# Performance work log

Measured on AMD Instinct MI355X. Metric: run time of the kernel, lower is better.

Reference implementation:

```python
import jax, jax.numpy as jnp
import numpy as np

DIM = 1024
HEADS = 16
HEAD_DIM = DIM // HEADS
NUM_FILTERS = 4
NUM_TAPS = 101
RES = 512

def setup_inputs() -> dict:
    key = jax.random.key(0)
    ks = jax.random.split(key, 5)
    B, S = 2, 2048
    x = jax.random.normal(ks[0], (B, S, DIM), dtype=jnp.float32)
    Wqkv = jax.random.normal(ks[1], (3 * DIM, DIM), dtype=jnp.float32) * (DIM ** -0.5)
    Wout = jax.random.normal(ks[2], (DIM, DIM), dtype=jnp.float32) * (DIM ** -0.5)
    Wpos = jax.random.normal(ks[3], (HEADS, NUM_FILTERS), dtype=jnp.float32) * 0.5
    coeffs = jax.random.normal(ks[4], (NUM_FILTERS, NUM_TAPS), dtype=jnp.float32) * 0.05
    return {"x": x, "Wqkv": Wqkv, "Wout": Wout, "Wpos": Wpos, "coeffs": coeffs}

def _fir_fft(c, sig):
    # c: (T,), sig: (R,) -> causal FFT convolution, first R samples
    R = sig.shape[0]
    L = R + c.shape[0] - 1
    out = jnp.fft.ifft(jnp.fft.fft(sig, n=L) * jnp.fft.fft(c, n=L)).real
    return out[:R]

def reference(x, Wqkv, Wout, Wpos, coeffs):
    B, S, D = x.shape
    scale = HEAD_DIM ** -0.5

    # filtered prototype table: (R, F)
    proto = jnp.linspace(0.0, 1.0, RES).astype(x.dtype)
    table = jax.vmap(_fir_fft, in_axes=(0, None))(coeffs, proto).T  # (R, F)

    # relative-distance index matrix (S, S), constants derived from static shape
    r = jnp.arange(S)
    rel = jnp.abs(r[None, :] - r[:, None]).astype(jnp.float32) / max(S - 1, 1)
    idx = jnp.clip(jnp.round(rel * (RES - 1)).astype(jnp.int32), 0, RES - 1)

    pos_feat = table[idx]                                   # (S, S, F)
    pos_bias = jnp.einsum('ijf,hf->hij', pos_feat, Wpos)    # (H, S, S)

    qkv = jnp.einsum('bsd,ed->bse', x, Wqkv)                # (B, S, 3D)
    q, k, v = jnp.split(qkv, 3, axis=-1)
    q = q.reshape(B, S, HEADS, HEAD_DIM)
    k = k.reshape(B, S, HEADS, HEAD_DIM)
    v = v.reshape(B, S, HEADS, HEAD_DIM)

    logits = jnp.einsum('bihd,bjhd->bhij', q, k) * scale + pos_bias[None]
    attn = jax.nn.softmax(logits, axis=-1)
    out = jnp.einsum('bhij,bjhd->bihd', attn, v).reshape(B, S, D)
    return jnp.einsum('bsd,ed->bse', out, Wout)
```

## Files before the change

### kernel.cpp

```cpp
#include <hip/hip_runtime.h>
#include <hip/hip_bf16.h>
#include <cstddef>

#define SEQ     2048
#define BATCH   2
#define DIMSZ   1024
#define HEADS   16
#define HDIM    64
#define E3      3072
#define RESN    512
#define NTAPS   101
#define NFILT   4
#define MROWS   (BATCH * SEQ)
#define LOG2E   1.44269504088896340736f

typedef __attribute__((ext_vector_type(8))) short bf16x8;
typedef __attribute__((ext_vector_type(4))) float f32x4;

__device__ __forceinline__ unsigned short f2bf(float f) {
  unsigned u = __float_as_uint(f);
  u += 0x7fffu + ((u >> 16) & 1u);
  return (unsigned short)(u >> 16);
}
__device__ __forceinline__ float bf2f(unsigned short h) {
  return __uint_as_float(((unsigned)h) << 16);
}
__device__ __forceinline__ void split2(float f, unsigned short& h, unsigned short& l) {
  h = f2bf(f);
  l = f2bf(f - bf2f(h));
}
__device__ __forceinline__ unsigned pkbf(float a, float b) {
  __hip_bfloat162 t = __float22bfloat162_rn(float2{a, b});
  union { __hip_bfloat162 h; unsigned u; } cv; cv.h = t;
  return cv.u;
}
__device__ __forceinline__ void async16(void* lds, const void* g) {
  __builtin_amdgcn_global_load_lds(
      (const __attribute__((address_space(1))) unsigned int*)g,
      (__attribute__((address_space(3))) unsigned int*)lds, 16, 0, 0);
}
#define EXP2(x) __builtin_amdgcn_exp2f(x)

__global__ __launch_bounds__(256) void cvt_bf16_kern(
    const float* __restrict__ src, unsigned short* __restrict__ dst, int n)
{
  const int i = (blockIdx.x * 256 + threadIdx.x) * 8;
  if (i >= n) return;
  const float4 a = *(const float4*)(src + i);
  const float4 b = *(const float4*)(src + i + 4);
  ushort4 p = {f2bf(a.x), f2bf(a.y), f2bf(a.z), f2bf(a.w)};
  ushort4 q = {f2bf(b.x), f2bf(b.y), f2bf(b.z), f2bf(b.w)};
  *(ushort4*)(dst + i)     = p;
  *(ushort4*)(dst + i + 4) = q;
}

__global__ __launch_bounds__(256) void split_pair_kern(
    const float* __restrict__ src, unsigned short* __restrict__ hi,
    unsigned short* __restrict__ lo, int n)
{
  const int i = (blockIdx.x * 256 + threadIdx.x) * 4;
  if (i >= n) return;
  const float4 a = *(const float4*)(src + i);
  ushort4 h, l;
  split2(a.x, h.x, l.x); split2(a.y, h.y, l.y);
  split2(a.z, h.z, l.z); split2(a.w, h.w, l.w);
  *(ushort4*)(hi + i) = h;
  *(ushort4*)(lo + i) = l;
}

__global__ __launch_bounds__(256) void pbias_kernel(
    const float* __restrict__ coeffs, const float* __restrict__ Wpos,
    float* __restrict__ pbias2)
{
  __shared__ float table[RESN][NFILT];
  const int h = blockIdx.x;
  const int tid = threadIdx.x;
  for (int rf = tid; rf < RESN * NFILT; rf += 256) {
    const int r = rf >> 2, f = rf & 3;
    const int tmax = r < (NTAPS - 1) ? r : (NTAPS - 1);
    float s = 0.f;
    for (int t = 0; t <= tmax; ++t)
      s += coeffs[f * NTAPS + t] * ((float)(r - t) * (1.0f / (float)(RESN - 1)));
    table[r][f] = s;
  }
  __syncthreads();
  float wp[NFILT];
#pragma unroll
  for (int f = 0; f < NFILT; ++f) wp[f] = Wpos[h * NFILT + f];
  for (int d = tid; d < SEQ; d += 256) {
    const float rel = (float)d / (float)(SEQ - 1);
    int idx = (int)rintf(rel * (float)(RESN - 1));
    idx = idx < 0 ? 0 : (idx > RESN - 1 ? RESN - 1 : idx);
    float s = 0.f;
#pragma unroll
    for (int f = 0; f < NFILT; ++f) s += table[idx][f] * wp[f];
    pbias2[h * SEQ + d] = s * LOG2E;
  }
}

__global__ __launch_bounds__(256, 4) void gemm_bf16(
    const unsigned short* __restrict__ A, const unsigned short* __restrict__ B,
    unsigned short* __restrict__ C, int M, int N, int K)
{
  __shared__ unsigned short As[2][128][32];
  __shared__ unsigned short Bs[2][128][32];
  const int tid = threadIdx.x;
  const int lane = tid & 63;
  const int w = tid >> 6, wm = w >> 1, wn = w & 1;
  const int c = lane & 15, G = lane >> 4;

  const int nwg = gridDim.x * gridDim.y;
  const int bid = blockIdx.y * gridDim.x + blockIdx.x;
  const int swz = (bid & 7) * (nwg >> 3) + (bid >> 3);
  const int bx = swz % gridDim.x, by = swz / gridDim.x;
  const int m0 = by * 128, n0 = bx * 128;

  const int srow = lane >> 2;
  const int scol = (lane & 3) << 3;
  const unsigned short* Ab = A + (size_t)m0 * K;
  const unsigned short* Bb = B + (size_t)n0 * K;

  f32x4 acc[4][4];
#pragma unroll
  for (int mf = 0; mf < 4; ++mf)
#pragma unroll
    for (int nf = 0; nf < 4; ++nf) acc[mf][nf] = (f32x4){0.f, 0.f, 0.f, 0.f};

  auto stage = [&](int buf, int k0) {
#pragma unroll
    for (int r = 0; r < 2; ++r) {
      const int chunk = r * 4 + w;
      const int row = (chunk << 4) + srow;
      async16(&As[buf][chunk << 4][0], Ab + (size_t)row * K + k0 + scol);
      async16(&Bs[buf][chunk << 4][0], Bb + (size_t)row * K + k0 + scol);
    }
  };

  stage(0, 0);
  __syncthreads();
  int cur = 0;
  const int NT = K >> 5;
  for (int t = 0; t < NT; ++t) {
    if (t + 1 < NT) stage(cur ^ 1, (t + 1) << 5);
    bf16x8 fa[4], fb[4];
#pragma unroll
    for (int mf = 0; mf < 4; ++mf)
      fa[mf] = *(const bf16x8*)&As[cur][wm * 64 + 16 * mf + c][8 * G];
#pragma unroll
    for (int nf = 0; nf < 4; ++nf)
      fb[nf] = *(const bf16x8*)&Bs[cur][wn * 64 + 16 * nf + c][8 * G];
#pragma unroll
    for (int nf = 0; nf < 4; ++nf)
#pragma unroll
      for (int mf = 0; mf < 4; ++mf)
        acc[mf][nf] = __builtin_amdgcn_mfma_f32_16x16x32_bf16(fa[mf], fb[nf], acc[mf][nf], 0, 0, 0);
    __syncthreads();
    cur ^= 1;
  }

#pragma unroll
  for (int mf = 0; mf < 4; ++mf)
#pragma unroll
    for (int nf = 0; nf < 4; ++nf)
#pragma unroll
      for (int r = 0; r < 4; ++r)
        C[(size_t)(m0 + wm * 64 + 16 * mf + 4 * G + r) * N + n0 + wn * 64 + 16 * nf + c] =
            f2bf(acc[mf][nf][r]);
}

__global__ __launch_bounds__(256, 4) void gemm_split3(
    const unsigned short* __restrict__ Ah, const unsigned short* __restrict__ Al,
    const unsigned short* __restrict__ Bh, const unsigned short* __restrict__ Bl,
    float* __restrict__ C, int M, int N, int K)
{
  __shared__ unsigned short AhS[2][64][32], AlS[2][64][32];
  __shared__ unsigned short BhS[2][64][32], BlS[2][64][32];
  const int tid = threadIdx.x;
  const int lane = tid & 63;
  const int w = tid >> 6, wm = w >> 1, wn = w & 1;
  const int c = lane & 15, G = lane >> 4;

  const int nwg = gridDim.x * gridDim.y;
  const int bid = blockIdx.y * gridDim.x + blockIdx.x;
  const int swz = (bid & 7) * (nwg >> 3) + (bid >> 3);
  const int bx = swz % gridDim.x, by = swz / gridDim.x;
  const int m0 = by * 64, n0 = bx * 64;

  const int srow = lane >> 2;
  const int scol = (lane & 3) << 3;

  f32x4 acc[2][2];
#pragma unroll
  for (int mf = 0; mf < 2; ++mf)
#pragma unroll
    for (int nf = 0; nf < 2; ++nf) acc[mf][nf] = (f32x4){0.f, 0.f, 0.f, 0.f};

  auto stage = [&](int buf, int k0) {
    const int arow = m0 + 16 * w + srow;
    const int brow = n0 + 16 * w + srow;
    async16(&AhS[buf][16 * w][0], Ah + (size_t)arow * K + k0 + scol);
    async16(&AlS[buf][16 * w][0], Al + (size_t)arow * K + k0 + scol);
    async16(&BhS[buf][16 * w][0], Bh + (size_t)brow * K + k0 + scol);
    async16(&BlS[buf][16 * w][0], Bl + (size_t)brow * K + k0 + scol);
  };

  stage(0, 0);
  __syncthreads();
  int cur = 0;
  const int NT = K >> 5;
  for (int t = 0; t < NT; ++t) {
    if (t + 1 < NT) stage(cur ^ 1, (t + 1) << 5);
    bf16x8 fah[2], fal[2], fbh[2], fbl[2];
#pragma unroll
    for (int mf = 0; mf < 2; ++mf) {
      fah[mf] = *(const bf16x8*)&AhS[cur][32 * wm + 16 * mf + c][8 * G];
      fal[mf] = *(const bf16x8*)&AlS[cur][32 * wm + 16 * mf + c][8 * G];
    }
#pragma unroll
    for (int nf = 0; nf < 2; ++nf) {
      fbh[nf] = *(const bf16x8*)&BhS[cur][32 * wn + 16 * nf + c][8 * G];
      fbl[nf] = *(const bf16x8*)&BlS[cur][32 * wn + 16 * nf + c][8 * G];
    }
#pragma unroll
    for (int nf = 0; nf < 2; ++nf)
#pragma unroll
      for (int mf = 0; mf < 2; ++mf) {
        acc[mf][nf] = __builtin_amdgcn_mfma_f32_16x16x32_bf16(fah[mf], fbh[nf], acc[mf][nf], 0, 0, 0);
        acc[mf][nf] = __builtin_amdgcn_mfma_f32_16x16x32_bf16(fah[mf], fbl[nf], acc[mf][nf], 0, 0, 0);
        acc[mf][nf] = __builtin_amdgcn_mfma_f32_16x16x32_bf16(fal[mf], fbh[nf], acc[mf][nf], 0, 0, 0);
      }
    __syncthreads();
    cur ^= 1;
  }

#pragma unroll
  for (int mf = 0; mf < 2; ++mf)
#pragma unroll
    for (int nf = 0; nf < 2; ++nf)
#pragma unroll
      for (int r = 0; r < 4; ++r)
        C[(size_t)(m0 + 32 * wm + 16 * mf + 4 * G + r) * N + n0 + 32 * wn + 16 * nf + c] =
            acc[mf][nf][r];
}

__global__ __launch_bounds__(256, 4) void attn_pure(
    const unsigned short* __restrict__ qkv,
    const float* __restrict__ pbias2,
    unsigned short* __restrict__ ao_hi,
    unsigned short* __restrict__ ao_lo)
{
  __shared__ unsigned short Kh[64][64];
  __shared__ unsigned short Vh[64][64];
  __shared__ unsigned short Ps[64][64];
  __shared__ float pb[SEQ];

  const int tid = threadIdx.x;
  const int lane = tid & 63;
  const int w = tid >> 6;
  const int c = lane & 15, G = lane >> 4;
  const int bh = blockIdx.y, b = bh >> 4, h = bh & 15;
  const int i0 = blockIdx.x * 64;
  const int i_glob = i0 + w * 16 + c;
  const float scale2 = 0.125f * LOG2E;

  for (int idx = tid * 4; idx < SEQ; idx += 1024)
    *(float4*)&pb[idx] = *(const float4*)(pbias2 + h * SEQ + idx);

  bf16x8 qb[2];
#pragma unroll
  for (int ks = 0; ks < 2; ++ks)
    qb[ks] = *(const bf16x8*)(qkv + (size_t)(b * SEQ + i_glob) * E3 + h * HDIM + 32 * ks + 8 * G);

  f32x4 oacc[4];
#pragma unroll
  for (int nf = 0; nf < 4; ++nf) oacc[nf] = (f32x4){0.f, 0.f, 0.f, 0.f};
  float mi = -1e30f, li = 0.f;

  const int vd8 = 8 * (tid & 7);
  const int vjp = 2 * (tid >> 3);
  const int klrow = lane >> 3;
  const int klsl  = lane & 7;

  for (int jt = 0; jt < SEQ / 64; ++jt) {
    const int j0 = jt * 64;
    const size_t rowK = (size_t)(b * SEQ + j0) * E3 + DIMSZ + h * HDIM;
    const size_t rowV = (size_t)(b * SEQ + j0) * E3 + 2 * DIMSZ + h * HDIM;

    const bf16x8 v0 = *(const bf16x8*)(qkv + rowV + (size_t)vjp * E3 + vd8);
    const bf16x8 v1 = *(const bf16x8*)(qkv + rowV + (size_t)(vjp + 1) * E3 + vd8);

    __syncthreads();

#pragma unroll
    for (int r = 0; r < 2; ++r) {
      const int chunk = r * 4 + w;
      const int krow = (chunk << 3) + klrow;
      const int ksl = klsl ^ (krow & 7);
      async16(&Kh[chunk << 3][0], qkv + rowK + (size_t)krow * E3 + 8 * ksl);
    }
#pragma unroll
    for (int e = 0; e < 8; ++e) {
      const int d = vd8 + e;
      const unsigned pk = (unsigned)(unsigned short)v0[e] |
                          ((unsigned)(unsigned short)v1[e] << 16);
      const int col = (((vjp >> 3) ^ (d & 7)) << 3) | (vjp & 7);
      *(unsigned*)&Vh[d][col] = pk;
    }
    __syncthreads();

    f32x4 st[4];
#pragma unroll
    for (int mf = 0; mf < 4; ++mf) st[mf] = (f32x4){0.f, 0.f, 0.f, 0.f};
#pragma unroll
    for (int ks = 0; ks < 2; ++ks)
#pragma unroll
      for (int mf = 0; mf < 4; ++mf) {
        const int sr = (4 * ks + G) ^ (c & 7);
        const bf16x8 ka = *(const bf16x8*)&Kh[16 * mf + c][8 * sr];
        st[mf] = __builtin_amdgcn_mfma_f32_16x16x32_bf16(ka, qb[ks], st[mf], 0, 0, 0);
      }

    float p[16];
    float rm = -1e30f;
#pragma unroll
    for (int mf = 0; mf < 4; ++mf)
#pragma unroll
      for (int r = 0; r < 4; ++r) {
        const int j = j0 + 16 * mf + 4 * G + r;
        const int d = i_glob > j ? i_glob - j : j - i_glob;
        const float lg = fmaf(st[mf][r], scale2, pb[d]);
        p[mf * 4 + r] = lg;
        rm = fmaxf(rm, lg);
      }
    rm = fmaxf(rm, __shfl_xor(rm, 16));
    rm = fmaxf(rm, __shfl_xor(rm, 32));
    const float newm = fmaxf(mi, rm);
    const float fr = EXP2(mi - newm);
    float rs = 0.f;
#pragma unroll
    for (int t = 0; t < 16; ++t) {
      p[t] = EXP2(p[t] - newm);
      rs += p[t];
    }
    rs += __shfl_xor(rs, 16);
    rs += __shfl_xor(rs, 32);
    li = li * fr + rs;
    mi = newm;
    float frr[4];
#pragma unroll
    for (int r = 0; r < 4; ++r) frr[r] = __shfl(fr, 20 * G + r);
#pragma unroll
    for (int nf = 0; nf < 4; ++nf)
#pragma unroll
      for (int r = 0; r < 4; ++r) oacc[nf][r] *= frr[r];

#pragma unroll
    for (int mf = 0; mf < 4; ++mf) {
      const int sw = (2 * mf + (G >> 1)) ^ (c & 7);
      uint2 pw = {pkbf(p[4 * mf + 0], p[4 * mf + 1]),
                  pkbf(p[4 * mf + 2], p[4 * mf + 3])};
      *(uint2*)&Ps[16 * w + c][8 * sw + 4 * (G & 1)] = pw;
    }

#pragma unroll
    for (int ks = 0; ks < 2; ++ks) {
      const int spr = (4 * ks + G) ^ (c & 7);
      const bf16x8 pa = *(const bf16x8*)&Ps[16 * w + c][8 * spr];
#pragma unroll
      for (int nf = 0; nf < 4; ++nf) {
        const int d = 16 * nf + c;
        const int sv = (4 * ks + G) ^ (d & 7);
        const bf16x8 vb = *(const bf16x8*)&Vh[d][8 * sv];
        oacc[nf] = __builtin_amdgcn_mfma_f32_16x16x32_bf16(pa, vb, oacc[nf], 0, 0, 0);
      }
    }
  }

  float rinv[4];
#pragma unroll
  for (int r = 0; r < 4; ++r) rinv[r] = 1.0f / __shfl(li, 20 * G + r);
#pragma unroll
  for (int nf = 0; nf < 4; ++nf)
#pragma unroll
    for (int r = 0; r < 4; ++r) {
      const float v = oacc[nf][r] * rinv[r];
      const size_t off = (size_t)(b * SEQ + i0 + 16 * w + 4 * G + r) * DIMSZ +
                         h * HDIM + 16 * nf + c;
      unsigned short vh, vl;
      split2(v, vh, vl);
      ao_hi[off] = vh;
      ao_lo[off] = vl;
    }
}

extern "C" void kernel_launch(void* const* d_in, const int* in_sizes, int n_in,
                              void* d_out, int out_size, void* d_ws, size_t ws_size,
                              hipStream_t stream) {
  const float* x      = (const float*)d_in[0];
  const float* Wqkv   = (const float*)d_in[1];
  const float* Wout   = (const float*)d_in[2];
  const float* Wpos   = (const float*)d_in[3];
  const float* coeffs = (const float*)d_in[4];
  float* out = (float*)d_out;

  unsigned short* qkv_bf  = (unsigned short*)d_ws;
  unsigned short* x_bf    = qkv_bf + (size_t)MROWS * E3;
  unsigned short* wqkv_bf = x_bf + (size_t)MROWS * DIMSZ;
  unsigned short* wout_h  = wqkv_bf + (size_t)E3 * DIMSZ;
  unsigned short* wout_l  = wout_h + (size_t)DIMSZ * DIMSZ;
  unsigned short* ao_h    = wout_l + (size_t)DIMSZ * DIMSZ;
  unsigned short* ao_l    = ao_h + (size_t)MROWS * DIMSZ;
  float* pbias2 = (float*)(ao_l + (size_t)MROWS * DIMSZ);

  const int nx = MROWS * DIMSZ;
  const int nw = E3 * DIMSZ;
  const int no = DIMSZ * DIMSZ;

  cvt_bf16_kern<<<nx / 2048, 256, 0, stream>>>(x, x_bf, nx);
  cvt_bf16_kern<<<nw / 2048, 256, 0, stream>>>(Wqkv, wqkv_bf, nw);
  split_pair_kern<<<no / 1024, 256, 0, stream>>>(Wout, wout_h, wout_l, no);
  pbias_kernel<<<HEADS, 256, 0, stream>>>(coeffs, Wpos, pbias2);

  dim3 g1(E3 / 128, MROWS / 128);
  gemm_bf16<<<g1, 256, 0, stream>>>(x_bf, wqkv_bf, qkv_bf, MROWS, E3, DIMSZ);

  dim3 g2(SEQ / 64, BATCH * HEADS);
  attn_pure<<<g2, 256, 0, stream>>>(qkv_bf, pbias2, ao_h, ao_l);

  dim3 g3(DIMSZ / 64, MROWS / 64);
  gemm_split3<<<g3, 256, 0, stream>>>(ao_h, ao_l, wout_h, wout_l, out, MROWS, DIMSZ, DIMSZ);
}
```

Before: 318.1 us.

## Enlarge output GEMM tile, keep P in registers, lazy softmax rescale

The output projection GEMM now uses 128x64 tiles, so each B fragment load is reused across four M fragments. The attention kernel drops the shared P buffer and repacks P into MFMA A-operand layout with permlane swaps. It also skips the online-softmax rescale when the running max grows by no more than 8, reads the position bias directly from global memory instead of staging it in LDS, and swizzles the block order. These changes aim to cut LDS traffic, syncs and rescale ALU work, at the cost of more registers and uncached gather loads of the bias.

```diff
diff --git a/kernel.cpp b/kernel.cpp
--- a/kernel.cpp
+++ b/kernel.cpp
@@ -173,7 +173,7 @@
     const unsigned short* __restrict__ Bh, const unsigned short* __restrict__ Bl,
     float* __restrict__ C, int M, int N, int K)
 {
-  __shared__ unsigned short AhS[2][64][32], AlS[2][64][32];
+  __shared__ unsigned short AhS[2][128][32], AlS[2][128][32];
   __shared__ unsigned short BhS[2][64][32], BlS[2][64][32];
   const int tid = threadIdx.x;
   const int lane = tid & 63;
@@ -184,24 +184,27 @@
   const int bid = blockIdx.y * gridDim.x + blockIdx.x;
   const int swz = (bid & 7) * (nwg >> 3) + (bid >> 3);
   const int bx = swz % gridDim.x, by = swz / gridDim.x;
-  const int m0 = by * 64, n0 = bx * 64;
+  const int m0 = by * 128, n0 = bx * 64;
 
   const int srow = lane >> 2;
   const int scol = (lane & 3) << 3;
 
-  f32x4 acc[2][2];
-#pragma unroll
-  for (int mf = 0; mf < 2; ++mf)
+  f32x4 acc[4][2];
+#pragma unroll
+  for (int mf = 0; mf < 4; ++mf)
 #pragma unroll
     for (int nf = 0; nf < 2; ++nf) acc[mf][nf] = (f32x4){0.f, 0.f, 0.f, 0.f};
 
   auto stage = [&](int buf, int k0) {
-    const int arow = m0 + 16 * w + srow;
-    const int brow = n0 + 16 * w + srow;
-    async16(&AhS[buf][16 * w][0], Ah + (size_t)arow * K + k0 + scol);
-    async16(&AlS[buf][16 * w][0], Al + (size_t)arow * K + k0 + scol);
-    async16(&BhS[buf][16 * w][0], Bh + (size_t)brow * K + k0 + scol);
-    async16(&BlS[buf][16 * w][0], Bl + (size_t)brow * K + k0 + scol);
+#pragma unroll
+    for (int r = 0; r < 2; ++r) {
+      const int rowA = r * 64 + 16 * w + srow;
+      async16(&AhS[buf][r * 64 + 16 * w][0], Ah + (size_t)(m0 + rowA) * K + k0 + scol);
+      async16(&AlS[buf][r * 64 + 16 * w][0], Al + (size_t)(m0 + rowA) * K + k0 + scol);
+    }
+    const int rowB = 16 * w + srow;
+    async16(&BhS[buf][16 * w][0], Bh + (size_t)(n0 + rowB) * K + k0 + scol);
+    async16(&BlS[buf][16 * w][0], Bl + (size_t)(n0 + rowB) * K + k0 + scol);
   };
 
   stage(0, 0);
@@ -210,36 +213,34 @@
   const int NT = K >> 5;
   for (int t = 0; t < NT; ++t) {
     if (t + 1 < NT) stage(cur ^ 1, (t + 1) << 5);
-    bf16x8 fah[2], fal[2], fbh[2], fbl[2];
-#pragma unroll
-    for (int mf = 0; mf < 2; ++mf) {
-      fah[mf] = *(const bf16x8*)&AhS[cur][32 * wm + 16 * mf + c][8 * G];
-      fal[mf] = *(const bf16x8*)&AlS[cur][32 * wm + 16 * mf + c][8 * G];
+    bf16x8 fah[4], fal[4];
+#pragma unroll
+    for (int mf = 0; mf < 4; ++mf) {
+      fah[mf] = *(const bf16x8*)&AhS[cur][64 * wm + 16 * mf + c][8 * G];
+      fal[mf] = *(const bf16x8*)&AlS[cur][64 * wm + 16 * mf + c][8 * G];
     }
 #pragma unroll
     for (int nf = 0; nf < 2; ++nf) {
-      fbh[nf] = *(const bf16x8*)&BhS[cur][32 * wn + 16 * nf + c][8 * G];
-      fbl[nf] = *(const bf16x8*)&BlS[cur][32 * wn + 16 * nf + c][8 * G];
-    }
-#pragma unroll
-    for (int nf = 0; nf < 2; ++nf)
-#pragma unroll
-      for (int mf = 0; mf < 2; ++mf) {
-        acc[mf][nf] = __builtin_amdgcn_mfma_f32_16x16x32_bf16(fah[mf], fbh[nf], acc[mf][nf], 0, 0, 0);
-        acc[mf][nf] = __builtin_amdgcn_mfma_f32_16x16x32_bf16(fah[mf], fbl[nf], acc[mf][nf], 0, 0, 0);
-        acc[mf][nf] = __builtin_amdgcn_mfma_f32_16x16x32_bf16(fal[mf], fbh[nf], acc[mf][nf], 0, 0, 0);
+      const bf16x8 fbh = *(const bf16x8*)&BhS[cur][32 * wn + 16 * nf + c][8 * G];
+      const bf16x8 fbl = *(const bf16x8*)&BlS[cur][32 * wn + 16 * nf + c][8 * G];
+#pragma unroll
+      for (int mf = 0; mf < 4; ++mf) {
+        acc[mf][nf] = __builtin_amdgcn_mfma_f32_16x16x32_bf16(fah[mf], fbh, acc[mf][nf], 0, 0, 0);
+        acc[mf][nf] = __builtin_amdgcn_mfma_f32_16x16x32_bf16(fah[mf], fbl, acc[mf][nf], 0, 0, 0);
+        acc[mf][nf] = __builtin_amdgcn_mfma_f32_16x16x32_bf16(fal[mf], fbh, acc[mf][nf], 0, 0, 0);
       }
+    }
     __syncthreads();
     cur ^= 1;
   }
 
 #pragma unroll
-  for (int mf = 0; mf < 2; ++mf)
+  for (int mf = 0; mf < 4; ++mf)
 #pragma unroll
     for (int nf = 0; nf < 2; ++nf)
 #pragma unroll
       for (int r = 0; r < 4; ++r)
-        C[(size_t)(m0 + 32 * wm + 16 * mf + 4 * G + r) * N + n0 + 32 * wn + 16 * nf + c] =
+        C[(size_t)(m0 + 64 * wm + 16 * mf + 4 * G + r) * N + n0 + 32 * wn + 16 * nf + c] =
             acc[mf][nf][r];
 }
 
@@ -251,20 +252,20 @@
 {
   __shared__ unsigned short Kh[64][64];
   __shared__ unsigned short Vh[64][64];
-  __shared__ unsigned short Ps[64][64];
-  __shared__ float pb[SEQ];
 
   const int tid = threadIdx.x;
   const int lane = tid & 63;
   const int w = tid >> 6;
   const int c = lane & 15, G = lane >> 4;
-  const int bh = blockIdx.y, b = bh >> 4, h = bh & 15;
-  const int i0 = blockIdx.x * 64;
+
+  const int bid = blockIdx.y * gridDim.x + blockIdx.x;
+  const int swz = (bid & 7) * 128 + (bid >> 3);
+  const int bh = swz >> 5, qblk = swz & 31;
+  const int b = bh >> 4, h = bh & 15;
+  const int i0 = qblk * 64;
   const int i_glob = i0 + w * 16 + c;
   const float scale2 = 0.125f * LOG2E;
-
-  for (int idx = tid * 4; idx < SEQ; idx += 1024)
-    *(float4*)&pb[idx] = *(const float4*)(pbias2 + h * SEQ + idx);
+  const float* pbh = pbias2 + h * SEQ;
 
   bf16x8 qb[2];
 #pragma unroll
@@ -276,7 +277,8 @@
   for (int nf = 0; nf < 4; ++nf) oacc[nf] = (f32x4){0.f, 0.f, 0.f, 0.f};
   float mi = -1e30f, li = 0.f;
 
-  const int vd8 = 8 * (tid & 7);
+  const int vk  = tid & 7;
+  const int vd8 = 8 * vk;
   const int vjp = 2 * (tid >> 3);
   const int klrow = lane >> 3;
   const int klsl  = lane & 7;
@@ -303,9 +305,20 @@
       const int d = vd8 + e;
       const unsigned pk = (unsigned)(unsigned short)v0[e] |
                           ((unsigned)(unsigned short)v1[e] << 16);
-      const int col = (((vjp >> 3) ^ (d & 7)) << 3) | (vjp & 7);
+      const int col = ((((vjp >> 3) ^ e ^ vk) & 7) << 3) | (vjp & 7);
       *(unsigned*)&Vh[d][col] = pk;
     }
+
+    float pbv[16];
+#pragma unroll
+    for (int mf = 0; mf < 4; ++mf)
+#pragma unroll
+      for (int r = 0; r < 4; ++r) {
+        const int j = j0 + 16 * mf + 4 * G + r;
+        const int d = i_glob > j ? i_glob - j : j - i_glob;
+        pbv[mf * 4 + r] = pbh[d];
+      }
+
     __syncthreads();
 
     f32x4 st[4];
@@ -323,57 +336,62 @@
     float p[16];
     float rm = -1e30f;
 #pragma unroll
-    for (int mf = 0; mf < 4; ++mf)
-#pragma unroll
-      for (int r = 0; r < 4; ++r) {
-        const int j = j0 + 16 * mf + 4 * G + r;
-        const int d = i_glob > j ? i_glob - j : j - i_glob;
-        const float lg = fmaf(st[mf][r], scale2, pb[d]);
-        p[mf * 4 + r] = lg;
-        rm = fmaxf(rm, lg);
-      }
+    for (int t = 0; t < 16; ++t) {
+      const float lg = fmaf(st[t >> 2][t & 3], scale2, pbv[t]);
+      p[t] = lg;
+      rm = fmaxf(rm, lg);
+    }
     rm = fmaxf(rm, __shfl_xor(rm, 16));
     rm = fmaxf(rm, __shfl_xor(rm, 32));
-    const float newm = fmaxf(mi, rm);
-    const float fr = EXP2(mi - newm);
+    const bool skip = __all(rm <= mi + 8.f);
+    if (!skip) {
+      const float newm = fmaxf(mi, rm);
+      const float fr = EXP2(mi - newm);
+      mi = newm;
+      float frr[4];
+#pragma unroll
+      for (int r = 0; r < 4; ++r) frr[r] = __shfl(fr, 20 * G + r);
+#pragma unroll
+      for (int nf = 0; nf < 4; ++nf)
+#pragma unroll
+        for (int r = 0; r < 4; ++r) oacc[nf][r] *= frr[r];
+      li *= fr;
+    }
     float rs = 0.f;
 #pragma unroll
     for (int t = 0; t < 16; ++t) {
-      p[t] = EXP2(p[t] - newm);
+      p[t] = EXP2(p[t] - mi);
       rs += p[t];
     }
     rs += __shfl_xor(rs, 16);
     rs += __shfl_xor(rs, 32);
-    li = li * fr + rs;
-    mi = newm;
-    float frr[4];
-#pragma unroll
-    for (int r = 0; r < 4; ++r) frr[r] = __shfl(fr, 20 * G + r);
-#pragma unroll
-    for (int nf = 0; nf < 4; ++nf)
-#pragma unroll
-      for (int r = 0; r < 4; ++r) oacc[nf][r] *= frr[r];
-
-#pragma unroll
-    for (int mf = 0; mf < 4; ++mf) {
-      const int sw = (2 * mf + (G >> 1)) ^ (c & 7);
-      uint2 pw = {pkbf(p[4 * mf + 0], p[4 * mf + 1]),
-                  pkbf(p[4 * mf + 2], p[4 * mf + 3])};
-      *(uint2*)&Ps[16 * w + c][8 * sw + 4 * (G & 1)] = pw;
-    }
-
+    li += rs;
+
+    bf16x8 pa[2];
 #pragma unroll
     for (int ks = 0; ks < 2; ++ks) {
-      const int spr = (4 * ks + G) ^ (c & 7);
-      const bf16x8 pa = *(const bf16x8*)&Ps[16 * w + c][8 * spr];
+      unsigned a0 = pkbf(p[8 * ks + 0], p[8 * ks + 1]);
+      unsigned a1 = pkbf(p[8 * ks + 2], p[8 * ks + 3]);
+      unsigned b0 = pkbf(p[8 * ks + 4], p[8 * ks + 5]);
+      unsigned b1 = pkbf(p[8 * ks + 6], p[8 * ks + 7]);
+      asm("v_permlane32_swap_b32 %0, %1" : "+v"(a0), "+v"(b0));
+      asm("v_permlane16_swap_b32 %0, %1" : "+v"(a0), "+v"(b0));
+      asm("v_permlane32_swap_b32 %0, %1" : "+v"(a1), "+v"(b1));
+      asm("v_permlane16_swap_b32 %0, %1" : "+v"(a1), "+v"(b1));
+      union { unsigned u[4]; bf16x8 v; } pw;
+      pw.u[0] = a0; pw.u[1] = a1; pw.u[2] = b0; pw.u[3] = b1;
+      pa[ks] = pw.v;
+    }
+
+#pragma unroll
+    for (int ks = 0; ks < 2; ++ks)
 #pragma unroll
       for (int nf = 0; nf < 4; ++nf) {
         const int d = 16 * nf + c;
-        const int sv = (4 * ks + G) ^ (d & 7);
+        const int sv = (4 * ks + G) ^ (c & 7) ^ ((2 * nf + (c >> 3)) & 7);
         const bf16x8 vb = *(const bf16x8*)&Vh[d][8 * sv];
-        oacc[nf] = __builtin_amdgcn_mfma_f32_16x16x32_bf16(pa, vb, oacc[nf], 0, 0, 0);
+        oacc[nf] = __builtin_amdgcn_mfma_f32_16x16x32_bf16(pa[ks], vb, oacc[nf], 0, 0, 0);
       }
-    }
   }
 
   float rinv[4];
@@ -427,6 +445,6 @@
   dim3 g2(SEQ / 64, BATCH * HEADS);
   attn_pure<<<g2, 256, 0, stream>>>(qkv_bf, pbias2, ao_h, ao_l);
 
-  dim3 g3(DIMSZ / 64, MROWS / 64);
+  dim3 g3(DIMSZ / 64, MROWS / 128);
   gemm_split3<<<g3, 256, 0, stream>>>(ao_h, ao_l, wout_h, wout_l, out, MROWS, DIMSZ, DIMSZ);
 }
```

Result: faster. 283.4 us (-10.9%).
